# Kernel optimization log

Measured on AMD Instinct MI355X. Metric: run time of the kernel, lower is better.

## Reference

```python
import jax, jax.numpy as jnp
import numpy as np

N_NODES = 100000
N_EDGES = 1600000
N_FEAT = 64
HIDDEN = 16


def setup_inputs() -> dict:
    key = jax.random.key(0)
    ks = jax.random.split(key, 10)
    x = jax.random.normal(ks[0], (N_NODES, N_FEAT), dtype=jnp.float32)
    edge_index = jax.random.randint(ks[1], (2, N_EDGES), 0, N_NODES, dtype=jnp.int64)
    As = jax.random.normal(ks[2], (2, N_EDGES), dtype=jnp.float32)
    ws_weights = jax.random.normal(ks[3], (2,), dtype=jnp.float32)
    Wl1 = jax.random.normal(ks[4], (N_FEAT, HIDDEN), dtype=jnp.float32) / np.sqrt(N_FEAT)
    bl1 = jnp.zeros((HIDDEN,), dtype=jnp.float32)
    Wr1 = jax.random.normal(ks[5], (N_FEAT, HIDDEN), dtype=jnp.float32) / np.sqrt(N_FEAT)
    Wl2 = jax.random.normal(ks[6], (HIDDEN, 1), dtype=jnp.float32) / np.sqrt(HIDDEN)
    bl2 = jnp.zeros((1,), dtype=jnp.float32)
    Wr2 = jax.random.normal(ks[7], (HIDDEN, 1), dtype=jnp.float32) / np.sqrt(HIDDEN)
    return {"x": x, "edge_index": edge_index, "As": As, "ws_weights": ws_weights,
            "Wl1": Wl1, "bl1": bl1, "Wr1": Wr1, "Wl2": Wl2, "bl2": bl2, "Wr2": Wr2}


def reference(x, edge_index, As, ws_weights, Wl1, bl1, Wr1, Wl2, bl2, Wr2):
    # WeightedSumLayer: weighted sum of per-edge weight vectors
    ewm = jnp.einsum('m,me->e', ws_weights, As)  # [E]
    # edge mask (nonzero weighted sum keeps the edge); instead of slicing to a
    # data-dependent edge count, zero out masked messages (same aggregation).
    mask = (ewm != 0).astype(x.dtype)  # [E]
    src, dst = edge_index[0], edge_index[1]
    n = x.shape[0]

    # SAGEConv layer 1 (aggr='sum'): out = lin_l(sum_j x_j) + lin_r(x)
    msg1 = x[src] * mask[:, None]                             # [E, F]
    agg1 = jax.ops.segment_sum(msg1, dst, num_segments=n)     # [N, F]
    h = jax.nn.relu(agg1 @ Wl1 + bl1 + x @ Wr1)               # [N, H]

    # SAGEConv layer 2
    msg2 = h[src] * mask[:, None]                             # [E, H]
    agg2 = jax.ops.segment_sum(msg2, dst, num_segments=n)     # [N, H]
    out = agg2 @ Wl2 + bl2 + h @ Wr2                          # [N, 1]
    return out
```

## Files before the change

### kernel.cpp

```cpp
#include <hip/hip_runtime.h>
#include <hip/hip_bf16.h>

constexpr int NN = 100000;
constexpr int NE = 1600000;
constexpr int NF = 64;
constexpr int NH = 16;

constexpr int NPB  = 128;
constexpr int LB   = 7;
constexpr int NBKT = (NN + NPB - 1) / NPB;
constexpr int CAP  = 2560;
constexpr int CHUNK = 4096;
constexpr int NBF   = (NE + CHUNK - 1) / CHUNK;
constexpr int NBLK_K1 = (NN + 255) / 256;
constexpr int FD = NBKT + 1;

constexpr int SMEM_BYTES = CHUNK * 4 + CHUNK * 4 + NBKT * 4 + FD * 4 + 256 * 4;

__device__ __forceinline__ float bf16_to_f32(unsigned short u) {
    return __uint_as_float(((unsigned int)u) << 16);
}
__device__ __forceinline__ unsigned short f32_to_bf16(float f) {
    __hip_bfloat16 hb = __float2bfloat16(f);
    return *reinterpret_cast<unsigned short*>(&hb);
}

__global__ __launch_bounds__(256)
void k_fused(const float* __restrict__ x,
             const float* __restrict__ Wl1,
             const float* __restrict__ Wr1,
             unsigned short* __restrict__ p,
             float* __restrict__ r,
             const int* __restrict__ ei, const float* __restrict__ As,
             const float* __restrict__ ws,
             unsigned int* __restrict__ gchunk, int* __restrict__ fdir)
{
    __shared__ __align__(16) char smem[SMEM_BYTES];
    int role = blockIdx.x & 1;
    int rb   = blockIdx.x >> 1;
    int tid  = threadIdx.x;

    if (role == 0) {
        float* sW = (float*)smem;
        for (int i = tid; i < NF * NH; i += 256) {
            sW[i]           = Wl1[i];
            sW[NF * NH + i] = Wr1[i];
        }
        __syncthreads();

        int n = rb * 256 + tid;
        if (n >= NN) return;

        float aL[NH], aR[NH];
#pragma unroll
        for (int j = 0; j < NH; ++j) { aL[j] = 0.f; aR[j] = 0.f; }

        const float4* xr = reinterpret_cast<const float4*>(x + (size_t)n * NF);
#pragma unroll
        for (int k4 = 0; k4 < NF / 4; ++k4) {
            float4 v = xr[k4];
            float xs[4] = {v.x, v.y, v.z, v.w};
#pragma unroll
            for (int t = 0; t < 4; ++t) {
                const float* wl = &sW[(k4 * 4 + t) * NH];
                const float* wr = &sW[NF * NH + (k4 * 4 + t) * NH];
#pragma unroll
                for (int j = 0; j < NH; ++j) {
                    aL[j] = fmaf(xs[t], wl[j], aL[j]);
                    aR[j] = fmaf(xs[t], wr[j], aR[j]);
                }
            }
        }

        unsigned int pu[8];
#pragma unroll
        for (int j2 = 0; j2 < 8; ++j2)
            pu[j2] = (unsigned int)f32_to_bf16(aL[2*j2]) |
                     ((unsigned int)f32_to_bf16(aL[2*j2+1]) << 16);
        uint4* pp = reinterpret_cast<uint4*>(p + (size_t)n * NH);
        pp[0] = make_uint4(pu[0], pu[1], pu[2], pu[3]);
        pp[1] = make_uint4(pu[4], pu[5], pu[6], pu[7]);

        float4* rp = reinterpret_cast<float4*>(r + (size_t)n * NH);
#pragma unroll
        for (int j4 = 0; j4 < NH / 4; ++j4)
            rp[j4] = make_float4(aR[j4*4], aR[j4*4+1], aR[j4*4+2], aR[j4*4+3]);
    } else {
        unsigned int* sw    = (unsigned int*)smem;
        unsigned int* srk   = sw + CHUNK;
        int*          lcnt  = (int*)(srk + CHUNK);
        int*          fscan = lcnt + NBKT;
        int*          tscan = fscan + FD;

        for (int i = tid; i < NBKT; i += 256) lcnt[i] = 0;
        __syncthreads();

        int base = rb * CHUNK;
        float w0 = ws[0], w1 = ws[1];

#pragma unroll
        for (int j = 0; j < CHUNK / 256; ++j) {
            int idx = j * 256 + tid;
            int e = base + idx;
            unsigned int rk = 0xFFFFFFFFu, w = 0;
            if (e < NE) {
                float ewm = w0 * As[e] + w1 * As[NE + e];
                if (ewm != 0.f) {
                    int dst = ei[NE + e];
                    int bk  = dst >> LB;
                    w  = ((unsigned)ei[e] << LB) | (unsigned)(dst & (NPB - 1));
                    int rank = atomicAdd(&lcnt[bk], 1);
                    rk = ((unsigned)bk << 12) | (unsigned)rank;
                }
            }
            sw[idx]  = w;
            srk[idx] = rk;
        }
        __syncthreads();

        {
            int loc[4]; int s = 0;
#pragma unroll
            for (int g = 0; g < 4; ++g) {
                int idx = tid * 4 + g;
                int v = (idx < NBKT) ? lcnt[idx] : 0;
                loc[g] = s; s += v;
            }
            tscan[tid] = s;
            __syncthreads();
            for (int off = 1; off < 256; off <<= 1) {
                int u = (tid >= off) ? tscan[tid - off] : 0;
                __syncthreads();
                tscan[tid] += u;
                __syncthreads();
            }
            int bse = (tid > 0) ? tscan[tid - 1] : 0;
#pragma unroll
            for (int g = 0; g < 4; ++g) {
                int idx = tid * 4 + g;
                if (idx < NBKT) fscan[idx] = bse + loc[g];
            }
            if (tid == 255) fscan[NBKT] = tscan[255];
        }
        __syncthreads();

        for (int i = tid; i < FD; i += 256)
            fdir[(size_t)rb * FD + i] = fscan[i];

#pragma unroll
        for (int j = 0; j < CHUNK / 256; ++j) {
            int idx = j * 256 + tid;
            unsigned int rk = srk[idx];
            if (rk != 0xFFFFFFFFu) {
                int pos = fscan[rk >> 12] + (int)(rk & 4095u);
                gchunk[(size_t)rb * CHUNK + pos] = sw[idx];
            }
        }
    }
}

__global__ __launch_bounds__(256)
void k_agg1(const int* __restrict__ fdir, const unsigned int* __restrict__ gchunk,
            unsigned int* __restrict__ bmem,
            const unsigned short* __restrict__ p, const float* __restrict__ r,
            const float* __restrict__ bl1, const float* __restrict__ Wl2,
            const float* __restrict__ bl2, const float* __restrict__ Wr2,
            float* __restrict__ q, float* __restrict__ out,
            int* __restrict__ gsoff)
{
    __shared__ unsigned int sbm[CAP];
    __shared__ unsigned int ssorted[CAP];
    __shared__ int fstart[NBF];
    __shared__ int foff[NBF + 1];
    __shared__ int tscan[256];
    __shared__ int hist[NPB];
    __shared__ int hscan[NPB];
    __shared__ int soff[NPB + 1];

    int b = blockIdx.x;
    int tid = threadIdx.x;
    if (tid < NPB) hist[tid] = 0;

    {
        int loc[2]; int s = 0;
#pragma unroll
        for (int g = 0; g < 2; ++g) {
            int f = tid * 2 + g;
            int sz = 0;
            if (f < NBF) {
                int s0 = fdir[(size_t)f * FD + b];
                int s1 = fdir[(size_t)f * FD + b + 1];
                fstart[f] = s0;
                sz = s1 - s0;
            }
            loc[g] = s; s += sz;
        }
        tscan[tid] = s;
        __syncthreads();
        for (int off = 1; off < 256; off <<= 1) {
            int u = (tid >= off) ? tscan[tid - off] : 0;
            __syncthreads();
            tscan[tid] += u;
            __syncthreads();
        }
        int bse = (tid > 0) ? tscan[tid - 1] : 0;
#pragma unroll
        for (int g = 0; g < 2; ++g) {
            int f = tid * 2 + g;
            if (f < NBF) foff[f] = bse + loc[g];
        }
        if (tid == 255) foff[NBF] = tscan[255];
    }
    __syncthreads();

    int cnt = min(foff[NBF], CAP);

    {
        int grp = tid >> 4, k = tid & 15;
        for (int f = grp; f < NBF; f += 16) {
            int o  = foff[f];
            int sz = foff[f + 1] - o;
            int s  = fstart[f];
            const unsigned int* src = gchunk + (size_t)f * CHUNK + s;
            int lim = min(sz, CAP - o);
            for (int j = k; j < lim; j += 16)
                sbm[o + j] = src[j];
        }
    }
    __syncthreads();

    int rk[CAP / 256];
#pragma unroll
    for (int j = 0; j < CAP / 256; ++j) {
        int i = j * 256 + tid;
        if (i < cnt)
            rk[j] = atomicAdd(&hist[sbm[i] & (NPB - 1)], 1);
    }
    __syncthreads();

    if (tid < NPB) hscan[tid] = hist[tid];
    __syncthreads();
    for (int off = 1; off < NPB; off <<= 1) {
        int u = (tid < NPB && tid >= off) ? hscan[tid - off] : 0;
        __syncthreads();
        if (tid < NPB) hscan[tid] += u;
        __syncthreads();
    }
    if (tid < NPB) soff[tid + 1] = hscan[tid];
    if (tid == 0) soff[0] = 0;
    __syncthreads();

#pragma unroll
    for (int j = 0; j < CAP / 256; ++j) {
        int i = j * 256 + tid;
        if (i < cnt) {
            unsigned int w = sbm[i];
            ssorted[soff[w & (NPB - 1)] + rk[j]] = w;
        }
    }
    __syncthreads();

    for (int i = tid; i < cnt; i += 256)
        bmem[(size_t)b * CAP + i] = ssorted[i];
    if (tid < NPB + 1)
        gsoff[(size_t)b * (NPB + 1) + tid] = soff[tid];

    int g = tid >> 4, k = tid & 15;
    int n0 = b * NPB;
#pragma unroll
    for (int jj = 0; jj < 8; ++jj) {
        int nl = g * 8 + jj;
        int s = soff[nl], e = soff[nl + 1];
        float a = 0.f;
        int i = s;
        for (; i + 3 < e; i += 4) {
            unsigned w0 = ssorted[i], w1 = ssorted[i+1], w2 = ssorted[i+2], w3 = ssorted[i+3];
            float v0 = bf16_to_f32(p[(size_t)(w0 >> LB) * NH + k]);
            float v1 = bf16_to_f32(p[(size_t)(w1 >> LB) * NH + k]);
            float v2 = bf16_to_f32(p[(size_t)(w2 >> LB) * NH + k]);
            float v3 = bf16_to_f32(p[(size_t)(w3 >> LB) * NH + k]);
            a += (v0 + v1) + (v2 + v3);
        }
        for (; i < e; ++i)
            a += bf16_to_f32(p[(size_t)(ssorted[i] >> LB) * NH + k]);

        int n = n0 + nl;
        if (n < NN) {
            float h = a + r[(size_t)n * NH + k] + bl1[k];
            h = h > 0.f ? h : 0.f;
            float qv = h * Wl2[k];
            float sv = h * Wr2[k];
#pragma unroll
            for (int m = 8; m >= 1; m >>= 1) {
                qv += __shfl_xor(qv, m);
                sv += __shfl_xor(sv, m);
            }
            if (k == 0) {
                q[n]   = qv;
                out[n] = sv + bl2[0];
            }
        }
    }
}

__global__ __launch_bounds__(256)
void k_agg2(const int* __restrict__ gsoff, const unsigned int* __restrict__ bmem,
            const float* __restrict__ q, float* __restrict__ out)
{
    int n = blockIdx.x * 256 + threadIdx.x;
    if (n >= NN) return;
    int b  = n >> LB;
    int dl = n & (NPB - 1);
    int s = gsoff[(size_t)b * (NPB + 1) + dl];
    int e = gsoff[(size_t)b * (NPB + 1) + dl + 1];
    const unsigned int* bm = bmem + (size_t)b * CAP;

    float a = 0.f;
    int i = s;
    for (; i + 3 < e; i += 4) {
        unsigned w0 = bm[i], w1 = bm[i+1], w2 = bm[i+2], w3 = bm[i+3];
        a += (q[w0 >> LB] + q[w1 >> LB]) + (q[w2 >> LB] + q[w3 >> LB]);
    }
    for (; i < e; ++i)
        a += q[bm[i] >> LB];
    out[n] += a;
}

extern "C" void kernel_launch(void* const* d_in, const int* in_sizes, int n_in,
                              void* d_out, int out_size, void* d_ws, size_t ws_size,
                              hipStream_t stream)
{
    const float* x   = (const float*)d_in[0];
    const int*   ei  = (const int*)  d_in[1];
    const float* As  = (const float*)d_in[2];
    const float* ws  = (const float*)d_in[3];
    const float* Wl1 = (const float*)d_in[4];
    const float* bl1 = (const float*)d_in[5];
    const float* Wr1 = (const float*)d_in[6];
    const float* Wl2 = (const float*)d_in[7];
    const float* bl2 = (const float*)d_in[8];
    const float* Wr2 = (const float*)d_in[9];
    float* out = (float*)d_out;

    unsigned short* p      = (unsigned short*)d_ws;
    float*          r      = (float*)(p + (size_t)NN * NH);
    float*          q      = r + (size_t)NN * NH;
    int*            gsoff  = (int*)(q + NN);
    int*            fdir   = gsoff + (size_t)NBKT * (NPB + 1);
    unsigned int*   gchunk = (unsigned int*)(fdir + (size_t)NBF * FD);
    unsigned int*   bmem   = gchunk + (size_t)NBF * CHUNK;

    int nblk = 2 * ((NBF > NBLK_K1) ? NBF : NBLK_K1);
    k_fused<<<nblk, 256, 0, stream>>>(x, Wl1, Wr1, p, r, ei, As, ws, gchunk, fdir);
    k_agg1<<<NBKT, 256, 0, stream>>>(fdir, gchunk, bmem, p, r, bl1, Wl2, bl2, Wr2,
                                     q, out, gsoff);
    k_agg2<<<(NN + 255) / 256, 256, 0, stream>>>(gsoff, bmem, q, out);
}
```

Before: 181.7 us.

## Double edge chunk size, use 512-thread blocks and recompute packed edges in scatter

The edge bucketing pass now works on chunks of 8192 edges with 512-thread blocks, which halves the number of chunks that the aggregation kernel must scan per bucket. To fit shared memory, the per-edge packed word is no longer staged; only a 16-bit rank is kept, and the scatter pass re-reads src/dst from global memory to rebuild the packed value. This trades extra global reads in the scatter for less shared memory, fewer chunk directories and a simpler one-entry-per-thread scan in k_agg1. The node projection role also moves to 512 threads per block.

```diff
diff --git a/kernel.cpp b/kernel.cpp
--- a/kernel.cpp
+++ b/kernel.cpp
@@ -10,12 +10,13 @@
 constexpr int LB   = 7;
 constexpr int NBKT = (NN + NPB - 1) / NPB;
 constexpr int CAP  = 2560;
-constexpr int CHUNK = 4096;
+constexpr int TB   = 512;
+constexpr int CHUNK = 8192;
 constexpr int NBF   = (NE + CHUNK - 1) / CHUNK;
-constexpr int NBLK_K1 = (NN + 255) / 256;
+constexpr int NBLK_K1 = (NN + TB - 1) / TB;
 constexpr int FD = NBKT + 1;
 
-constexpr int SMEM_BYTES = CHUNK * 4 + CHUNK * 4 + NBKT * 4 + FD * 4 + 256 * 4;
+constexpr int SMEM_BYTES = CHUNK * 2 + NBKT * 4 + FD * 4 + TB * 4;
 
 __device__ __forceinline__ float bf16_to_f32(unsigned short u) {
     return __uint_as_float(((unsigned int)u) << 16);
@@ -25,7 +26,7 @@
     return *reinterpret_cast<unsigned short*>(&hb);
 }
 
-__global__ __launch_bounds__(256)
+__global__ __launch_bounds__(TB)
 void k_fused(const float* __restrict__ x,
              const float* __restrict__ Wl1,
              const float* __restrict__ Wr1,
@@ -42,13 +43,13 @@
 
     if (role == 0) {
         float* sW = (float*)smem;
-        for (int i = tid; i < NF * NH; i += 256) {
+        for (int i = tid; i < NF * NH; i += TB) {
             sW[i]           = Wl1[i];
             sW[NF * NH + i] = Wr1[i];
         }
         __syncthreads();
 
-        int n = rb * 256 + tid;
+        int n = rb * TB + tid;
         if (n >= NN) return;
 
         float aL[NH], aR[NH];
@@ -86,49 +87,42 @@
         for (int j4 = 0; j4 < NH / 4; ++j4)
             rp[j4] = make_float4(aR[j4*4], aR[j4*4+1], aR[j4*4+2], aR[j4*4+3]);
     } else {
-        unsigned int* sw    = (unsigned int*)smem;
-        unsigned int* srk   = sw + CHUNK;
-        int*          lcnt  = (int*)(srk + CHUNK);
-        int*          fscan = lcnt + NBKT;
-        int*          tscan = fscan + FD;
-
-        for (int i = tid; i < NBKT; i += 256) lcnt[i] = 0;
+        unsigned short* srk  = (unsigned short*)smem;
+        int* lcnt  = (int*)(smem + CHUNK * 2);
+        int* fscan = lcnt + NBKT;
+        int* tscan = fscan + FD;
+
+        for (int i = tid; i < NBKT; i += TB) lcnt[i] = 0;
         __syncthreads();
 
         int base = rb * CHUNK;
         float w0 = ws[0], w1 = ws[1];
 
 #pragma unroll
-        for (int j = 0; j < CHUNK / 256; ++j) {
-            int idx = j * 256 + tid;
+        for (int j = 0; j < CHUNK / TB; ++j) {
+            int idx = j * TB + tid;
             int e = base + idx;
-            unsigned int rk = 0xFFFFFFFFu, w = 0;
+            unsigned short rk = 0xFFFFu;
             if (e < NE) {
                 float ewm = w0 * As[e] + w1 * As[NE + e];
-                if (ewm != 0.f) {
-                    int dst = ei[NE + e];
-                    int bk  = dst >> LB;
-                    w  = ((unsigned)ei[e] << LB) | (unsigned)(dst & (NPB - 1));
-                    int rank = atomicAdd(&lcnt[bk], 1);
-                    rk = ((unsigned)bk << 12) | (unsigned)rank;
-                }
-            }
-            sw[idx]  = w;
+                if (ewm != 0.f)
+                    rk = (unsigned short)atomicAdd(&lcnt[ei[NE + e] >> LB], 1);
+            }
             srk[idx] = rk;
         }
         __syncthreads();
 
         {
-            int loc[4]; int s = 0;
-#pragma unroll
-            for (int g = 0; g < 4; ++g) {
-                int idx = tid * 4 + g;
+            int loc[2]; int s = 0;
+#pragma unroll
+            for (int g = 0; g < 2; ++g) {
+                int idx = tid * 2 + g;
                 int v = (idx < NBKT) ? lcnt[idx] : 0;
                 loc[g] = s; s += v;
             }
             tscan[tid] = s;
             __syncthreads();
-            for (int off = 1; off < 256; off <<= 1) {
+            for (int off = 1; off < TB; off <<= 1) {
                 int u = (tid >= off) ? tscan[tid - off] : 0;
                 __syncthreads();
                 tscan[tid] += u;
@@ -136,24 +130,27 @@
             }
             int bse = (tid > 0) ? tscan[tid - 1] : 0;
 #pragma unroll
-            for (int g = 0; g < 4; ++g) {
-                int idx = tid * 4 + g;
+            for (int g = 0; g < 2; ++g) {
+                int idx = tid * 2 + g;
                 if (idx < NBKT) fscan[idx] = bse + loc[g];
             }
-            if (tid == 255) fscan[NBKT] = tscan[255];
-        }
-        __syncthreads();
-
-        for (int i = tid; i < FD; i += 256)
+            if (tid == TB - 1) fscan[NBKT] = tscan[TB - 1];
+        }
+        __syncthreads();
+
+        for (int i = tid; i < FD; i += TB)
             fdir[(size_t)rb * FD + i] = fscan[i];
 
 #pragma unroll
-        for (int j = 0; j < CHUNK / 256; ++j) {
-            int idx = j * 256 + tid;
-            unsigned int rk = srk[idx];
-            if (rk != 0xFFFFFFFFu) {
-                int pos = fscan[rk >> 12] + (int)(rk & 4095u);
-                gchunk[(size_t)rb * CHUNK + pos] = sw[idx];
+        for (int j = 0; j < CHUNK / TB; ++j) {
+            int idx = j * TB + tid;
+            unsigned short rk = srk[idx];
+            if (rk != 0xFFFFu) {
+                int e   = base + idx;
+                int dst = ei[NE + e];
+                int bk  = dst >> LB;
+                gchunk[(size_t)rb * CHUNK + fscan[bk] + rk] =
+                    ((unsigned)ei[e] << LB) | (unsigned)(dst & (NPB - 1));
             }
         }
     }
@@ -182,20 +179,14 @@
     if (tid < NPB) hist[tid] = 0;
 
     {
-        int loc[2]; int s = 0;
-#pragma unroll
-        for (int g = 0; g < 2; ++g) {
-            int f = tid * 2 + g;
-            int sz = 0;
-            if (f < NBF) {
-                int s0 = fdir[(size_t)f * FD + b];
-                int s1 = fdir[(size_t)f * FD + b + 1];
-                fstart[f] = s0;
-                sz = s1 - s0;
-            }
-            loc[g] = s; s += sz;
-        }
-        tscan[tid] = s;
+        int sz = 0;
+        if (tid < NBF) {
+            int s0 = fdir[(size_t)tid * FD + b];
+            int s1 = fdir[(size_t)tid * FD + b + 1];
+            fstart[tid] = s0;
+            sz = s1 - s0;
+        }
+        tscan[tid] = sz;
         __syncthreads();
         for (int off = 1; off < 256; off <<= 1) {
             int u = (tid >= off) ? tscan[tid - off] : 0;
@@ -203,12 +194,7 @@
             tscan[tid] += u;
             __syncthreads();
         }
-        int bse = (tid > 0) ? tscan[tid - 1] : 0;
-#pragma unroll
-        for (int g = 0; g < 2; ++g) {
-            int f = tid * 2 + g;
-            if (f < NBF) foff[f] = bse + loc[g];
-        }
+        if (tid < NBF) foff[tid] = tscan[tid] - sz;
         if (tid == 255) foff[NBF] = tscan[255];
     }
     __syncthreads();
@@ -351,7 +337,7 @@
     unsigned int*   bmem   = gchunk + (size_t)NBF * CHUNK;
 
     int nblk = 2 * ((NBF > NBLK_K1) ? NBF : NBLK_K1);
-    k_fused<<<nblk, 256, 0, stream>>>(x, Wl1, Wr1, p, r, ei, As, ws, gchunk, fdir);
+    k_fused<<<nblk, TB, 0, stream>>>(x, Wl1, Wr1, p, r, ei, As, ws, gchunk, fdir);
     k_agg1<<<NBKT, 256, 0, stream>>>(fdir, gchunk, bmem, p, r, bl1, Wl2, bl2, Wr2,
                                      q, out, gsoff);
     k_agg2<<<(NN + 255) / 256, 256, 0, stream>>>(gsoff, bmem, q, out);
```

Result: faster. 174.1 us (-4.2%).
